# Optimization experiments

Measured on AMD Instinct MI355X. Metric: run time of the kernel, lower is better.

Reference implementation:

```python
import jax, jax.numpy as jnp
import numpy as np

NUM_HEADS = 16  # config.num_attention_heads


def setup_inputs() -> dict:
    key = jax.random.key(0)
    k0, k1, k2 = jax.random.split(key, 3)
    B, S, D = 2, 2048, 2048
    hd = D // NUM_HEADS  # 128
    hidden_states = jax.random.normal(k0, (B, S, D), dtype=jnp.float32)
    c_attn_w = jax.random.normal(k1, (D + 2 * hd, D), dtype=jnp.float32) * 0.02
    c_attn_b = jnp.zeros((D + 2 * hd,), dtype=jnp.float32)
    c_proj_w = jax.random.normal(k2, (D, D), dtype=jnp.float32) * 0.02
    c_proj_b = jnp.zeros((D,), dtype=jnp.float32)
    return {
        "hidden_states": hidden_states,
        "c_attn_w": c_attn_w,
        "c_attn_b": c_attn_b,
        "c_proj_w": c_proj_w,
        "c_proj_b": c_proj_b,
    }


def reference(hidden_states, c_attn_w, c_attn_b, c_proj_w, c_proj_b):
    B, S, D = hidden_states.shape
    H = NUM_HEADS
    hd = D // H
    scale = hd ** -0.5

    # fused QKV projection: [B,S,D] -> [B,S,D+2*hd]
    qkv = hidden_states @ c_attn_w.T + c_attn_b
    # multi-query split: per-head Q, single shared K and V
    q = qkv[..., :D].reshape(B, S, H, hd)        # [B,S,H,hd]
    k = qkv[..., D:D + hd]                       # [B,S,hd]
    v = qkv[..., D + hd:]                        # [B,S,hd]

    # attention scores (full matrix materialized, like the baddbmm path)
    scores = jnp.einsum('bqhd,bkd->bhqk', q, k) * scale  # [B,H,S,S]
    causal = jnp.tril(jnp.ones((S, S), dtype=bool))
    scores = jnp.where(causal, scores, jnp.finfo(scores.dtype).min)
    attn = jax.nn.softmax(scores, axis=-1)

    # context: shared V broadcast across heads
    ctx = jnp.einsum('bhqk,bkd->bqhd', attn, v).reshape(B, S, D)
    out = ctx @ c_proj_w.T + c_proj_b
    return out
```

## Files before the change

kernel.cpp:

```cpp
#include <hip/hip_runtime.h>
#include <hip/hip_bf16.h>
#include <math.h>

typedef unsigned short u16;
typedef __attribute__((ext_vector_type(8))) __bf16 bf16x8;
typedef __attribute__((ext_vector_type(4))) float f32x4;

__device__ inline u16 f2bf(float f) {
  union { float f; unsigned u; } x; x.f = f;
  unsigned r = x.u + 0x7fffu + ((x.u >> 16) & 1u);
  return (u16)(r >> 16);
}

__device__ inline unsigned cvtpk(float lo, float hi) {
  unsigned r;
  asm("v_cvt_pk_bf16_f32 %0, %1, %2" : "=v"(r) : "v"(lo), "v"(hi));
  return r;
}

__device__ inline float fexp2(float x) {
  float r;
  asm("v_exp_f32 %0, %1" : "=v"(r) : "v"(x));
  return r;
}

__device__ inline void async16(const void* g, void* l) {
  __builtin_amdgcn_global_load_lds(
      (const __attribute__((address_space(1))) void*)g,
      (__attribute__((address_space(3))) void*)l, 16, 0, 0);
}

__global__ __launch_bounds__(256) void cast3_kernel(
    const float* __restrict__ hs, const float* __restrict__ aw,
    const float* __restrict__ pw, u16* __restrict__ hs_o,
    u16* __restrict__ aw_o, u16* __restrict__ pw_o) {
  int blk = blockIdx.x;
  const float* in;
  u16* out;
  int i;
  if (blk < 4096) {
    in = hs; out = hs_o; i = blk * 256 + threadIdx.x;
  } else if (blk < 6400) {
    in = aw; out = aw_o; i = (blk - 4096) * 256 + threadIdx.x;
  } else {
    in = pw; out = pw_o; i = (blk - 6400) * 256 + threadIdx.x;
  }
#pragma unroll
  for (int p = 0; p < 2; ++p) {
    int q = i * 2 + p;
    float4 v = ((const float4*)in)[q];
    u16 o0 = f2bf(v.x), o1 = f2bf(v.y), o2 = f2bf(v.z), o3 = f2bf(v.w);
    unsigned lo = (unsigned)o0 | ((unsigned)o1 << 16);
    unsigned hi = (unsigned)o2 | ((unsigned)o3 << 16);
    ((uint2*)out)[q] = make_uint2(lo, hi);
  }
}

template <bool BF16OUT>
__global__ __launch_bounds__(256) void gemm_bt(
    const u16* __restrict__ A, const u16* __restrict__ Bw,
    const float* __restrict__ bias, void* __restrict__ Cout,
    u16* __restrict__ vtout, int M, int N, int K, int qcols, float qscale) {
  __shared__ u16 As[2][128 * 64];
  __shared__ u16 Bs[2][128 * 64];
  const int t = threadIdx.x;
  const int w = t >> 6;
  const int lane = t & 63;
  const int lq = lane >> 4, lr = lane & 15;

  int bx = blockIdx.x, by = blockIdx.y;
  const int gx = gridDim.x, gy = gridDim.y;
  if ((gx & 1) == 0 && (gy & 3) == 0) {
    const int cw = gx >> 1, ch = gy >> 2;
    int id = by * gx + bx;
    int xcd = id & 7, j = id >> 3;
    bx = (xcd & 1) * cw + j % cw;
    by = (xcd >> 1) * ch + j / cw;
  }

  const long brow = (long)by * 128;
  const long bcol = (long)bx * 128;
  const int wr = (w >> 1) * 64, wc = (w & 1) * 64;
  f32x4 acc[4][4] = {};

  int rA[4], cA[4];
#pragma unroll
  for (int it = 0; it < 4; ++it) {
    int ci = it * 256 + t;
    rA[it] = ci >> 3;
    cA[it] = (ci & 7) ^ (rA[it] & 7);
  }

  char* const AsB = (char*)&As[0][0];
  char* const BsB = (char*)&Bs[0][0];

  auto stage = [&](int buf, int kt) {
    char* ad = AsB + buf * 16384;
    char* bd = BsB + buf * 16384;
#pragma unroll
    for (int it = 0; it < 4; ++it) {
      const u16* srcA = A + (brow + rA[it]) * (long)K + kt + cA[it] * 8;
      async16(srcA, ad + (it * 256 + w * 64) * 16);
      const u16* srcB = Bw + (bcol + rA[it]) * (long)K + kt + cA[it] * 8;
      async16(srcB, bd + (it * 256 + w * 64) * 16);
    }
  };

  const int swz = ((lr & 4) << 4) + ((lq << 4) ^ ((lr & 3) << 4));
  const int aB0 = (wr + lr) * 128 + swz;
  const int bB0 = (wc + lr) * 128 + swz;
  const char* const a00 = AsB + aB0;
  const char* const a01 = AsB + (aB0 ^ 64);
  const char* const a10 = AsB + 16384 + aB0;
  const char* const a11 = AsB + 16384 + (aB0 ^ 64);
  const char* const b00 = BsB + bB0;
  const char* const b01 = BsB + (bB0 ^ 64);
  const char* const b10 = BsB + 16384 + bB0;
  const char* const b11 = BsB + 16384 + (bB0 ^ 64);

  auto computeK = [&](const char* a0, const char* a1, const char* b0,
                      const char* b1) {
    bf16x8 af[4], bfr[4];
#pragma unroll
    for (int m = 0; m < 4; ++m) af[m] = *(const bf16x8*)(a0 + m * 2048);
#pragma unroll
    for (int n = 0; n < 4; ++n) bfr[n] = *(const bf16x8*)(b0 + n * 2048);
#pragma unroll
    for (int m = 0; m < 4; ++m)
#pragma unroll
      for (int n = 0; n < 4; ++n)
        acc[m][n] = __builtin_amdgcn_mfma_f32_16x16x32_bf16(
            af[m], bfr[n], acc[m][n], 0, 0, 0);
#pragma unroll
    for (int m = 0; m < 4; ++m) af[m] = *(const bf16x8*)(a1 + m * 2048);
#pragma unroll
    for (int n = 0; n < 4; ++n) bfr[n] = *(const bf16x8*)(b1 + n * 2048);
#pragma unroll
    for (int m = 0; m < 4; ++m)
#pragma unroll
      for (int n = 0; n < 4; ++n)
        acc[m][n] = __builtin_amdgcn_mfma_f32_16x16x32_bf16(
            af[m], bfr[n], acc[m][n], 0, 0, 0);
  };

  stage(0, 0);
  __syncthreads();

  for (int kt = 0; kt < K; kt += 128) {
    if (kt + 64 < K) stage(1, kt + 64);
    computeK(a00, a01, b00, b01);
    __syncthreads();
    if (kt + 128 < K) stage(0, kt + 128);
    computeK(a10, a11, b10, b11);
    __syncthreads();
  }

#pragma unroll
  for (int m = 0; m < 4; ++m) {
    long row0 = brow + wr + m * 16 + lq * 4;
#pragma unroll
    for (int n = 0; n < 4; ++n) {
      long col = bcol + wc + n * 16 + lr;
      float bv = bias[col];
      float cs = (col < qcols) ? qscale : 1.f;
#pragma unroll
      for (int j = 0; j < 4; ++j) {
        float v = (acc[m][n][j] + bv) * cs;
        if (BF16OUT)
          ((u16*)Cout)[(row0 + j) * N + col] = f2bf(v);
        else
          ((float*)Cout)[(row0 + j) * N + col] = v;
      }
    }
  }

  if (BF16OUT && vtout != nullptr && bcol == 2176) {
    const int bb = (int)(brow >> 11);
    const int s0 = (int)(brow & 2047) + wr + lq * 4;
#pragma unroll
    for (int m = 0; m < 4; ++m)
#pragma unroll
      for (int n = 0; n < 4; ++n) {
        int d = wc + n * 16 + lr;
        float bv = bias[2176 + d];
        union { u16 h[4]; uint2 u; } pk;
#pragma unroll
        for (int j = 0; j < 4; ++j) pk.h[j] = f2bf(acc[m][n][j] + bv);
        *(uint2*)(vtout + ((size_t)bb * 128 + d) * 2048 + s0 + m * 16) = pk.u;
      }
  }
}

__global__ __launch_bounds__(256, 2) void attn_kernel(
    const u16* __restrict__ qkv, const u16* __restrict__ vt,
    u16* __restrict__ ctx) {
  __shared__ u16 Kl[2][64 * 136];
  __shared__ u16 Vl[2][128 * 72];

  const int t = threadIdx.x;
  const int w = t >> 6;
  const int lane = t & 63;
  const int lq = lane >> 4, lr = lane & 15;
  const int lkey = lq * 4;
  const int kbase8 = lq << 3;
  const int bid = blockIdx.x;
  const int qtid = bid >> 5;
  const int qt = (qtid < 8) ? (15 - qtid) : (qtid - 8);
  const int hb = bid & 31;
  const int h = hb & 15;
  const int b = hb >> 4;
  const int s0w = qt * 128 + w * 32;
  const size_t qb = (size_t)b * 2048 * 2304;

  bf16x8 qg[2][4];
#pragma unroll
  for (int s = 0; s < 2; ++s)
#pragma unroll
    for (int kc = 0; kc < 4; ++kc)
      qg[s][kc] = *(const bf16x8*)(qkv + qb +
                                   (size_t)(s0w + s * 16 + lr) * 2304 +
                                   h * 128 + kc * 32 + lq * 8);

  const u16* kp[5];
  const u16* vp[5];
#pragma unroll
  for (int ii = 0; ii < 5; ++ii) {
    int I = 4 * ii + w;
    {
      int pp = I * 1024 + lane * 16;
      int row = pp / 272;
      int rem = pp - row * 272;
      int ch = (rem < 256) ? (rem >> 4) : 0;
      if (row > 63) row = 63;
      int g = row >> 4, lqr = row & 15;
      int key = ((g & 1) << 5) + ((lqr >> 2) << 3) + ((g >> 1) << 2) +
                (lqr & 3);
      kp[ii] = qkv + qb + (size_t)key * 2304 + 2048 + ch * 8;
    }
    {
      int pp = I * 1024 + lane * 16;
      int row = pp / 144;
      int rem = pp - row * 144;
      int ch = (rem < 128) ? (rem >> 4) : 0;
      if (row > 127) row = 127;
      vp[ii] = vt + ((size_t)b * 128 + row) * 2048 + ch * 8;
    }
  }
  char* const KlB = (char*)&Kl[0][0];
  char* const VlB = (char*)&Vl[0][0];

  auto stage = [&](int buf) {
    char* kd = KlB + buf * 17408;
    char* vd = VlB + buf * 18432;
#pragma unroll
    for (int ii = 0; ii < 5; ++ii) {
      int I = 4 * ii + w;
      if (I < 17) {
        async16(kp[ii], kd + I * 1024);
        kp[ii] += 64 * 2304;
      }
    }
#pragma unroll
    for (int ii = 0; ii < 5; ++ii) {
      int I = 4 * ii + w;
      if (I < 18) {
        async16(vp[ii], vd + I * 1024);
        vp[ii] += 64;
      }
    }
  };

  const int loK = lr * 272 + lq * 16;
  const int loV = lr * 144 + lq * 16;

  float mreg[2] = {-INFINITY, -INFINITY};
  float lreg[2] = {0.f, 0.f};
  f32x4 o[2][8] = {};
  const int ntiles = 2 * qt + 2;

  stage(0);
  __syncthreads();

  int cur = 0;
  for (int j2 = 0; j2 < ntiles; ++j2) {
    const int kvb = j2 * 64;
    if (j2 + 1 < ntiles) stage(cur ^ 1);
    if (kvb <= s0w + 31) {
      const char* KL = KlB + cur * 17408 + loK;
      const char* VL = VlB + cur * 18432 + loV;
      const bool maskT = (kvb + 63 > s0w);

      f32x4 sc[2][4] = {};
#pragma unroll
      for (int g = 0; g < 4; ++g)
#pragma unroll
        for (int kc = 0; kc < 4; ++kc) {
          bf16x8 kf = *(const bf16x8*)(KL + g * 4352 + kc * 64);
          sc[0][g] = __builtin_amdgcn_mfma_f32_16x16x32_bf16(kf, qg[0][kc],
                                                             sc[0][g], 0, 0, 0);
          sc[1][g] = __builtin_amdgcn_mfma_f32_16x16x32_bf16(kf, qg[1][kc],
                                                             sc[1][g], 0, 0, 0);
        }

      bf16x8 vf[16];
#pragma unroll
      for (int n = 0; n < 8; ++n) {
        vf[2 * n] = *(const bf16x8*)(VL + n * 2304);
        vf[2 * n + 1] = *(const bf16x8*)(VL + n * 2304 + 64);
      }

#pragma unroll
      for (int s = 0; s < 2; ++s) {
        float vv[16];
#pragma unroll
        for (int uu = 0; uu < 16; ++uu) vv[uu] = sc[s][uu >> 2][uu & 3];
        if (maskT) {
          const int qrel = s0w + s * 16 + lr - kvb - kbase8;
#pragma unroll
          for (int g = 0; g < 4; ++g)
#pragma unroll
            for (int r = 0; r < 4; ++r)
              if (((g & 1) << 5) + ((g >> 1) << 2) + r > qrel)
                vv[g * 4 + r] = -INFINITY;
        }
        float mx = vv[0];
#pragma unroll
        for (int uu = 1; uu < 16; ++uu) mx = fmaxf(mx, vv[uu]);
        mx = fmaxf(mx, __shfl_xor(mx, 16));
        mx = fmaxf(mx, __shfl_xor(mx, 32));
        float mn = mreg[s];
        if (__any(mx > mn + 8.f)) {
          float mu = fmaxf(mn, mx);
          float alpha = fexp2(mn - mu);
          mreg[s] = mu;
          mn = mu;
          lreg[s] *= alpha;
          float a0 = __shfl(alpha, lkey + 0);
          float a1 = __shfl(alpha, lkey + 1);
          float a2 = __shfl(alpha, lkey + 2);
          float a3 = __shfl(alpha, lkey + 3);
#pragma unroll
          for (int n = 0; n < 8; ++n) {
            o[s][n][0] *= a0;
            o[s][n][1] *= a1;
            o[s][n][2] *= a2;
            o[s][n][3] *= a3;
          }
        }
        float e[16];
        float rs = 0.f;
#pragma unroll
        for (int uu = 0; uu < 16; ++uu) {
          e[uu] = fexp2(vv[uu] - mn);
          rs += e[uu];
        }
        lreg[s] += rs;
        bf16x8 pa0, pa1;
        {
          union { unsigned uw[4]; bf16x8 v; } pk;
          pk.uw[0] = cvtpk(e[0], e[1]);
          pk.uw[1] = cvtpk(e[2], e[3]);
          pk.uw[2] = cvtpk(e[8], e[9]);
          pk.uw[3] = cvtpk(e[10], e[11]);
          pa0 = pk.v;
          pk.uw[0] = cvtpk(e[4], e[5]);
          pk.uw[1] = cvtpk(e[6], e[7]);
          pk.uw[2] = cvtpk(e[12], e[13]);
          pk.uw[3] = cvtpk(e[14], e[15]);
          pa1 = pk.v;
        }
#pragma unroll
        for (int n = 0; n < 8; ++n) {
          o[s][n] = __builtin_amdgcn_mfma_f32_16x16x32_bf16(pa0, vf[2 * n],
                                                            o[s][n], 0, 0, 0);
          o[s][n] = __builtin_amdgcn_mfma_f32_16x16x32_bf16(pa1, vf[2 * n + 1],
                                                            o[s][n], 0, 0, 0);
        }
      }
    }
    __syncthreads();
    cur ^= 1;
  }

#pragma unroll
  for (int s = 0; s < 2; ++s) {
    float lsum = lreg[s];
    lsum += __shfl_xor(lsum, 16);
    lsum += __shfl_xor(lsum, 32);
    float inv = 1.f / lsum;
    float iv[4];
    iv[0] = __shfl(inv, lkey + 0);
    iv[1] = __shfl(inv, lkey + 1);
    iv[2] = __shfl(inv, lkey + 2);
    iv[3] = __shfl(inv, lkey + 3);
#pragma unroll
    for (int r = 0; r < 4; ++r) {
      size_t rowoff =
          ((size_t)b * 2048 + s0w + s * 16 + lkey + r) * 2048 + h * 128;
#pragma unroll
      for (int n = 0; n < 8; ++n)
        ctx[rowoff + n * 16 + lr] = f2bf(o[s][n][r] * iv[r]);
    }
  }
}

extern "C" void kernel_launch(void* const* d_in, const int* in_sizes, int n_in,
                              void* d_out, int out_size, void* d_ws,
                              size_t ws_size, hipStream_t stream) {
  (void)in_sizes; (void)n_in; (void)out_size; (void)ws_size;
  const float* hs = (const float*)d_in[0];
  const float* attn_w = (const float*)d_in[1];
  const float* attn_b = (const float*)d_in[2];
  const float* proj_w = (const float*)d_in[3];
  const float* proj_b = (const float*)d_in[4];
  float* out = (float*)d_out;

  u16* hs_b = (u16*)d_ws;
  u16* aw_b = hs_b + (size_t)4096 * 2048;
  u16* pw_b = aw_b + (size_t)2304 * 2048;
  u16* qkv_b = pw_b + (size_t)2048 * 2048;
  u16* vt_b = qkv_b + (size_t)4096 * 2304;
  u16* ctx_b = vt_b + (size_t)2 * 128 * 2048;

  const float qscale = 0.08838834764831845f * 1.4426950408889634f;

  cast3_kernel<<<8448, 256, 0, stream>>>(hs, attn_w, proj_w, hs_b, aw_b,
                                         pw_b);

  gemm_bt<true><<<dim3(18, 32), 256, 0, stream>>>(hs_b, aw_b, attn_b, qkv_b,
                                                  vt_b, 4096, 2304, 2048,
                                                  2048, qscale);
  attn_kernel<<<512, 256, 0, stream>>>(qkv_b, vt_b, ctx_b);
  gemm_bt<false><<<dim3(16, 32), 256, 0, stream>>>(ctx_b, pw_b, proj_b, out,
                                                   nullptr, 4096, 2048, 2048,
                                                   0, 1.f);
}
```

Baseline: 172.7 us.

## Split long causal attention query tiles across two blocks and merge partials

The eight longest query tiles per head now have their KV range divided between two blocks, each writing unnormalized partial outputs plus per-row max and sum to workspace. A new combine kernel merges the two halves with log-sum-exp weights. The shorter tiles run unsplit as before. This evens out work across the 768 blocks to cut tail imbalance from causal masking, at the cost of an extra kernel launch, workspace traffic, and bf16 rounding of the partials.

```diff
diff --git a/kernel.cpp b/kernel.cpp
--- a/kernel.cpp
+++ b/kernel.cpp
@@ -10,6 +10,11 @@
   union { float f; unsigned u; } x; x.f = f;
   unsigned r = x.u + 0x7fffu + ((x.u >> 16) & 1u);
   return (u16)(r >> 16);
+}
+
+__device__ inline float bf2f(u16 h) {
+  union { unsigned u; float f; } x; x.u = ((unsigned)h) << 16;
+  return x.f;
 }
 
 __device__ inline unsigned cvtpk(float lo, float hi) {
@@ -193,7 +198,7 @@
 
 __global__ __launch_bounds__(256, 2) void attn_kernel(
     const u16* __restrict__ qkv, const u16* __restrict__ vt,
-    u16* __restrict__ ctx) {
+    u16* __restrict__ ctx, u16* __restrict__ pws) {
   __shared__ u16 Kl[2][64 * 136];
   __shared__ u16 Vl[2][128 * 72];
 
@@ -204,9 +209,26 @@
   const int lkey = lq * 4;
   const int kbase8 = lq << 3;
   const int bid = blockIdx.x;
-  const int qtid = bid >> 5;
-  const int qt = (qtid < 8) ? (15 - qtid) : (qtid - 8);
-  const int hb = bid & 31;
+
+  int qt, j0, j1, hb;
+  bool split;
+  if (bid < 512) {
+    int u = bid >> 6;
+    int half = (bid >> 5) & 1;
+    hb = bid & 31;
+    qt = 15 - u;
+    int T = 2 * qt + 2, T0 = T >> 1;
+    j0 = half ? T0 : 0;
+    j1 = half ? T : T0;
+    split = true;
+  } else {
+    int u2 = (bid - 512) >> 5;
+    hb = bid & 31;
+    qt = 7 - u2;
+    j0 = 0;
+    j1 = 2 * qt + 2;
+    split = false;
+  }
   const int h = hb & 15;
   const int b = hb >> 4;
   const int s0w = qt * 128 + w * 32;
@@ -235,7 +257,7 @@
       int g = row >> 4, lqr = row & 15;
       int key = ((g & 1) << 5) + ((lqr >> 2) << 3) + ((g >> 1) << 2) +
                 (lqr & 3);
-      kp[ii] = qkv + qb + (size_t)key * 2304 + 2048 + ch * 8;
+      kp[ii] = qkv + qb + (size_t)(key + j0 * 64) * 2304 + 2048 + ch * 8;
     }
     {
       int pp = I * 1024 + lane * 16;
@@ -243,7 +265,7 @@
       int rem = pp - row * 144;
       int ch = (rem < 128) ? (rem >> 4) : 0;
       if (row > 127) row = 127;
-      vp[ii] = vt + ((size_t)b * 128 + row) * 2048 + ch * 8;
+      vp[ii] = vt + ((size_t)b * 128 + row) * 2048 + j0 * 64 + ch * 8;
     }
   }
   char* const KlB = (char*)&Kl[0][0];
@@ -276,15 +298,14 @@
   float mreg[2] = {-INFINITY, -INFINITY};
   float lreg[2] = {0.f, 0.f};
   f32x4 o[2][8] = {};
-  const int ntiles = 2 * qt + 2;
 
   stage(0);
   __syncthreads();
 
   int cur = 0;
-  for (int j2 = 0; j2 < ntiles; ++j2) {
+  for (int j2 = j0; j2 < j1; ++j2) {
     const int kvb = j2 * 64;
-    if (j2 + 1 < ntiles) stage(cur ^ 1);
+    if (j2 + 1 < j1) stage(cur ^ 1);
     if (kvb <= s0w + 31) {
       const char* KL = KlB + cur * 17408 + loK;
       const char* VL = VlB + cur * 18432 + loV;
@@ -382,25 +403,96 @@
     cur ^= 1;
   }
 
-#pragma unroll
-  for (int s = 0; s < 2; ++s) {
-    float lsum = lreg[s];
-    lsum += __shfl_xor(lsum, 16);
-    lsum += __shfl_xor(lsum, 32);
-    float inv = 1.f / lsum;
-    float iv[4];
-    iv[0] = __shfl(inv, lkey + 0);
-    iv[1] = __shfl(inv, lkey + 1);
-    iv[2] = __shfl(inv, lkey + 2);
-    iv[3] = __shfl(inv, lkey + 3);
-#pragma unroll
-    for (int r = 0; r < 4; ++r) {
-      size_t rowoff =
-          ((size_t)b * 2048 + s0w + s * 16 + lkey + r) * 2048 + h * 128;
-#pragma unroll
-      for (int n = 0; n < 8; ++n)
-        ctx[rowoff + n * 16 + lr] = f2bf(o[s][n][r] * iv[r]);
-    }
+  if (split) {
+    u16* const po = pws + (size_t)bid * 16896;
+    float* const pml = (float*)(po + 16384);
+#pragma unroll
+    for (int s = 0; s < 2; ++s) {
+      float lsum = lreg[s];
+      lsum += __shfl_xor(lsum, 16);
+      lsum += __shfl_xor(lsum, 32);
+      if (lq == 0) {
+        pml[w * 32 + s * 16 + lr] = mreg[s];
+        pml[128 + w * 32 + s * 16 + lr] = lsum;
+      }
+#pragma unroll
+      for (int r = 0; r < 4; ++r) {
+        int row = w * 32 + s * 16 + lkey + r;
+#pragma unroll
+        for (int n = 0; n < 8; ++n)
+          po[row * 128 + n * 16 + lr] = f2bf(o[s][n][r]);
+      }
+    }
+  } else {
+#pragma unroll
+    for (int s = 0; s < 2; ++s) {
+      float lsum = lreg[s];
+      lsum += __shfl_xor(lsum, 16);
+      lsum += __shfl_xor(lsum, 32);
+      float inv = 1.f / lsum;
+      float iv[4];
+      iv[0] = __shfl(inv, lkey + 0);
+      iv[1] = __shfl(inv, lkey + 1);
+      iv[2] = __shfl(inv, lkey + 2);
+      iv[3] = __shfl(inv, lkey + 3);
+#pragma unroll
+      for (int r = 0; r < 4; ++r) {
+        size_t rowoff =
+            ((size_t)b * 2048 + s0w + s * 16 + lkey + r) * 2048 + h * 128;
+#pragma unroll
+        for (int n = 0; n < 8; ++n)
+          ctx[rowoff + n * 16 + lr] = f2bf(o[s][n][r] * iv[r]);
+      }
+    }
+  }
+}
+
+__global__ __launch_bounds__(256) void combine_kernel(
+    const u16* __restrict__ pws, u16* __restrict__ ctx) {
+  const int bid = blockIdx.x;
+  const int u = bid >> 5, hb = bid & 31;
+  const int h = hb & 15, b = hb >> 4;
+  const int qt = 15 - u;
+  const u16* const p0 = pws + (size_t)(u * 64 + hb) * 16896;
+  const u16* const p1 = pws + (size_t)(u * 64 + 32 + hb) * 16896;
+  const float* const ml0 = (const float*)(p0 + 16384);
+  const float* const ml1 = (const float*)(p1 + 16384);
+
+  __shared__ float f0s[128], f1s[128];
+  const int t = threadIdx.x;
+  if (t < 128) {
+    float m0 = ml0[t], l0 = ml0[128 + t];
+    float m1 = ml1[t], l1 = ml1[128 + t];
+    float M = fmaxf(m0, m1);
+    float w0 = fexp2(m0 - M), w1 = fexp2(m1 - M);
+    float L = l0 * w0 + l1 * w1;
+    f0s[t] = w0 / L;
+    f1s[t] = w1 / L;
+  }
+  __syncthreads();
+
+  const int row = t >> 1, dh = (t & 1) * 64;
+  const float f0 = f0s[row], f1 = f1s[row];
+  const uint4* r0 = (const uint4*)(p0 + row * 128 + dh);
+  const uint4* r1 = (const uint4*)(p1 + row * 128 + dh);
+  uint4* dst =
+      (uint4*)(ctx + ((size_t)b * 2048 + qt * 128 + row) * 2048 + h * 128 + dh);
+#pragma unroll
+  for (int j = 0; j < 8; ++j) {
+    uint4 A = r0[j], B = r1[j];
+    const unsigned* pa = (const unsigned*)&A;
+    const unsigned* pb = (const unsigned*)&B;
+    uint4 O;
+    unsigned* po = (unsigned*)&O;
+#pragma unroll
+    for (int k = 0; k < 4; ++k) {
+      float v0 = bf2f((u16)(pa[k] & 0xffff)) * f0 +
+                 bf2f((u16)(pb[k] & 0xffff)) * f1;
+      float v1 = bf2f((u16)(pa[k] >> 16)) * f0 +
+                 bf2f((u16)(pb[k] >> 16)) * f1;
+      po[k] = (unsigned)f2bf(v0) | ((unsigned)f2bf(v1) << 16);
+    }
+    dst[j] = O;
   }
 }
 
@@ -421,6 +513,7 @@
   u16* qkv_b = pw_b + (size_t)2048 * 2048;
   u16* vt_b = qkv_b + (size_t)4096 * 2304;
   u16* ctx_b = vt_b + (size_t)2 * 128 * 2048;
+  u16* pws = ctx_b + (size_t)4096 * 2048;
 
   const float qscale = 0.08838834764831845f * 1.4426950408889634f;
 
@@ -430,7 +523,8 @@
   gemm_bt<true><<<dim3(18, 32), 256, 0, stream>>>(hs_b, aw_b, attn_b, qkv_b,
                                                   vt_b, 4096, 2304, 2048,
                                                   2048, qscale);
-  attn_kernel<<<512, 256, 0, stream>>>(qkv_b, vt_b, ctx_b);
+  attn_kernel<<<768, 256, 0, stream>>>(qkv_b, vt_b, ctx_b, pws);
+  combine_kernel<<<256, 256, 0, stream>>>(pws, ctx_b);
   gemm_bt<false><<<dim3(16, 32), 256, 0, stream>>>(ctx_b, pw_b, proj_b, out,
                                                    nullptr, 4096, 2048, 2048,
                                                    0, 1.f);
```

After: 184.3 us. +6.7%, slower.
